# Performance work log

Measured on AMD Instinct MI355X. Metric: run time of the kernel, lower is better.

The kernel has to match this reference:

```python
import jax, jax.numpy as jnp
import numpy as np

QMAX = 127.0
QMIN = -128.0
THRESHOLD = 5e-07

def setup_inputs() -> dict:
    key = jax.random.key(0)
    k1, k2, k3 = jax.random.split(key, 3)
    B, S, Din, Dout = 4, 2048, 4096, 4096
    x = jax.random.normal(k1, (B, S, Din), dtype=jnp.float32)
    # Emulate QuantizedLinear.__init__: per-output-channel symmetric int8 weight quant
    w_fp = jax.random.normal(k2, (Dout, Din), dtype=jnp.float32) * 0.02
    w_scale = jnp.clip(jnp.max(jnp.abs(w_fp), axis=1, keepdims=True), THRESHOLD, None) / QMAX  # [Dout,1]
    weight = jnp.round(w_fp / w_scale)  # int8-valued, stored float32, [Dout, Din]
    weight_scale = w_scale.reshape(1, 1, Dout)  # [1,1,Dout]
    bias = jax.random.normal(k3, (Dout,), dtype=jnp.float32) * 0.01
    return {"x": x, "weight": weight, "weight_scale": weight_scale, "bias": bias}

def reference(x, weight, weight_scale, bias):
    # Dynamic per-tensor activation quantization (act_quant=True, no fixed range)
    fp_min = jnp.min(x)
    fp_max = jnp.max(x)
    scale = (fp_max - fp_min) / (QMAX - QMIN)
    zero_point = jnp.clip(jnp.round(QMIN - fp_min / scale), QMIN, QMAX)
    q_input = jnp.round(x / scale + zero_point)  # int8-valued float
    # F.linear(q_input - zp, weight): [B,S,Din] x [Dout,Din]^T -> [B,S,Dout]
    y = jnp.einsum('bsd,od->bso', q_input - zero_point, weight)
    y = y * scale * weight_scale  # dequant epilogue (weight_scale broadcasts [1,1,Dout])
    return y + bias
```

## Files before the change

kernel.cpp:

```cpp
#include <hip/hip_runtime.h>
#include <hip/hip_bf16.h>
#include <stdint.h>

typedef __attribute__((ext_vector_type(4))) int i32x4;

#define K_DIM 4096
#define M_DIM 8192
#define N_DIM 4096

#define BM 256
#define BN 256
#define BKB 128
#define K_TILES (K_DIM / BKB)
#define GITERS (K_TILES / 2)

__device__ __forceinline__ void gload_lds16(const void* g, void* l) {
    __builtin_amdgcn_global_load_lds(
        (__attribute__((address_space(1))) void*)(void*)g,
        (__attribute__((address_space(3))) void*)(void*)l,
        16, 0, 0);
}

__global__ void mmcw_kernel(const float* __restrict__ x, long n4,
                            float* __restrict__ partials,
                            const float* __restrict__ w,
                            signed char* __restrict__ Wq,
                            int* __restrict__ rowsum) {
    if (blockIdx.x < 1024) {
        const float4* x4 = (const float4*)x;
        float mn = 1e30f, mx = -1e30f;
        long stride = (long)1024 * blockDim.x;
        for (long i = (long)blockIdx.x * blockDim.x + threadIdx.x; i < n4; i += stride) {
            float4 v = x4[i];
            mn = fminf(mn, fminf(fminf(v.x, v.y), fminf(v.z, v.w)));
            mx = fmaxf(mx, fmaxf(fmaxf(v.x, v.y), fmaxf(v.z, v.w)));
        }
        #pragma unroll
        for (int off = 32; off; off >>= 1) {
            mn = fminf(mn, __shfl_down(mn, off));
            mx = fmaxf(mx, __shfl_down(mx, off));
        }
        __shared__ float smn[4], smx[4];
        int wid = threadIdx.x >> 6, lane = threadIdx.x & 63;
        if (lane == 0) { smn[wid] = mn; smx[wid] = mx; }
        __syncthreads();
        if (threadIdx.x == 0) {
            mn = fminf(fminf(smn[0], smn[1]), fminf(smn[2], smn[3]));
            mx = fmaxf(fmaxf(smx[0], smx[1]), fmaxf(smx[2], smx[3]));
            partials[blockIdx.x] = mn;
            partials[1024 + blockIdx.x] = mx;
        }
    } else {
        int row = (blockIdx.x - 1024) * 4 + (threadIdx.x >> 6);
        int lane = threadIdx.x & 63;
        const float4* src = (const float4*)(w + (long)row * K_DIM);
        uint4* dst = (uint4*)(Wq + (long)row * K_DIM);
        float s = 0.f;
        #pragma unroll
        for (int k = 0; k < 4; k++) {
            int u = k * 64 + lane;
            unsigned wrd[4];
            #pragma unroll
            for (int j = 0; j < 4; j++) {
                float4 v = src[u * 4 + j];
                float e[4] = {v.x, v.y, v.z, v.w};
                unsigned word = 0;
                #pragma unroll
                for (int b = 0; b < 4; b++) {
                    int iv = (int)e[b];
                    s += e[b];
                    word |= ((unsigned)iv & 0xffu) << (8 * b);
                }
                wrd[j] = word;
            }
            uint4 o; o.x = wrd[0]; o.y = wrd[1]; o.z = wrd[2]; o.w = wrd[3];
            dst[u] = o;
        }
        #pragma unroll
        for (int off = 32; off; off >>= 1) s += __shfl_down(s, off);
        if (lane == 0) rowsum[row] = (int)s;
    }
}

__global__ void quantize_kernel(const float* __restrict__ x,
                                const float* __restrict__ partials,
                                uint4* __restrict__ q, long n16) {
    float mn = 1e30f, mx = -1e30f;
    for (int i = threadIdx.x; i < 1024; i += 256) {
        mn = fminf(mn, partials[i]);
        mx = fmaxf(mx, partials[1024 + i]);
    }
    #pragma unroll
    for (int off = 32; off; off >>= 1) {
        mn = fminf(mn, __shfl_down(mn, off));
        mx = fmaxf(mx, __shfl_down(mx, off));
    }
    __shared__ float smn[4], smx[4];
    int wid = threadIdx.x >> 6, lane = threadIdx.x & 63;
    if (lane == 0) { smn[wid] = mn; smx[wid] = mx; }
    __syncthreads();
    mn = fminf(fminf(smn[0], smn[1]), fminf(smn[2], smn[3]));
    mx = fmaxf(fmaxf(smx[0], smx[1]), fmaxf(smx[2], smx[3]));
    float scale = (mx - mn) / 255.0f;
    float zp = rintf(-128.0f - mn / scale);
    zp = fminf(fmaxf(zp, -128.0f), 127.0f);

    long stride = (long)gridDim.x * blockDim.x;
    for (long i = (long)blockIdx.x * blockDim.x + threadIdx.x; i < n16; i += stride) {
        const float4* xp = (const float4*)x + i * 4;
        unsigned wrd[4];
        #pragma unroll
        for (int w = 0; w < 4; w++) {
            float4 v = xp[w];
            float e[4] = {v.x, v.y, v.z, v.w};
            unsigned word = 0;
            #pragma unroll
            for (int j = 0; j < 4; j++) {
                float qf = rintf(e[j] / scale + zp);
                qf = fminf(fmaxf(qf, -128.0f), 127.0f);
                int iq = (int)qf;
                word |= ((unsigned)iq & 0xffu) << (8 * j);
            }
            wrd[w] = word;
        }
        uint4 o; o.x = wrd[0]; o.y = wrd[1]; o.z = wrd[2]; o.w = wrd[3];
        q[i] = o;
    }
}

__global__ __launch_bounds__(512, 2) void gemm_kernel(
    const signed char* __restrict__ A,
    const signed char* __restrict__ W,
    const float* __restrict__ partials,
    const int* __restrict__ rowsum,
    const float* __restrict__ wscale,
    const float* __restrict__ bias,
    float* __restrict__ C) {
    extern __shared__ char lds[];
    char* As = lds;
    char* Bs = lds + 65536;

    int nwg = gridDim.x;
    int cpx = nwg >> 3;
    int bid = blockIdx.x;
    int wg = (bid & 7) * cpx + (bid >> 3);
    int tm = wg >> 4;
    int tn = wg & 15;
    int m0 = tm * BM, n0 = tn * BN;

    int t = threadIdx.x;
    int wid = t >> 6, lane = t & 63;
    int wr = wid >> 2, wc = wid & 3;
    int lr = lane & 15, lk = lane >> 4;
    int ksw0 = (lk ^ (lr & 7)) * 16;
    int ksw1 = ((4 + lk) ^ (lr & 7)) * 16;

    int R0 = t >> 3;
    int csw = ((t & 7) ^ ((t >> 3) & 7)) * 16;
    const signed char* aSrc = A + (long)(m0 + R0) * K_DIM + csw;
    const signed char* bSrc = W + (long)(n0 + ((R0 >> 5) << 6) + (R0 & 31)) * K_DIM + csw;
    int ldd = t * 16;

#define STAGE_A(BUF, UN, KT) do { \
    const signed char* _s = aSrc + (long)(UN) * 64 * K_DIM + (long)(KT) * BKB; \
    char* _d = As + (BUF) * 32768 + (UN) * 16384 + ldd; \
    gload_lds16(_s, _d); \
    gload_lds16(_s + (long)128 * K_DIM, _d + 8192); } while (0)

#define STAGE_B(BUF, UN, KT) do { \
    const signed char* _s = bSrc + (long)(UN) * 32 * K_DIM + (long)(KT) * BKB; \
    char* _d = Bs + (BUF) * 32768 + (UN) * 16384 + ldd; \
    gload_lds16(_s, _d); \
    gload_lds16(_s + (long)128 * K_DIM, _d + 8192); } while (0)

#define READ_A(BUF, MH) do { \
    const char* _p = As + (BUF) * 32768 + (MH) * 16384 + (wr * 64 + lr) * 128; \
    _Pragma("unroll") \
    for (int _mm = 0; _mm < 4; ++_mm) { \
        a[_mm * 2]     = *(const i32x4*)(_p + _mm * 2048 + ksw0); \
        a[_mm * 2 + 1] = *(const i32x4*)(_p + _mm * 2048 + ksw1); } } while (0)

#define READ_B(BUF, NH, BR) do { \
    const char* _p = Bs + (BUF) * 32768 + (NH) * 16384 + (wc * 32 + lr) * 128; \
    _Pragma("unroll") \
    for (int _nn = 0; _nn < 2; ++_nn) { \
        BR[_nn * 2]     = *(const i32x4*)(_p + _nn * 2048 + ksw0); \
        BR[_nn * 2 + 1] = *(const i32x4*)(_p + _nn * 2048 + ksw1); } } while (0)

#define MFMA_QUAD(MH, NH, BR) do { \
    _Pragma("unroll") \
    for (int _mm = 0; _mm < 4; ++_mm) \
    _Pragma("unroll") \
    for (int _nn = 0; _nn < 2; ++_nn) { \
        acc[(MH) * 4 + _mm][(NH) * 2 + _nn] = __builtin_amdgcn_mfma_i32_16x16x64_i8( \
            a[_mm * 2], BR[_nn * 2], acc[(MH) * 4 + _mm][(NH) * 2 + _nn], 0, 0, 0); \
        acc[(MH) * 4 + _mm][(NH) * 2 + _nn] = __builtin_amdgcn_mfma_i32_16x16x64_i8( \
            a[_mm * 2 + 1], BR[_nn * 2 + 1], acc[(MH) * 4 + _mm][(NH) * 2 + _nn], 0, 0, 0); } } while (0)

#define BAR()   asm volatile("s_barrier" ::: "memory")
#define LGKM0() asm volatile("s_waitcnt lgkmcnt(0)" ::: "memory")
#define LGKM8() asm volatile("s_waitcnt lgkmcnt(8)" ::: "memory")
#define VM6()   asm volatile("s_waitcnt vmcnt(6)" ::: "memory")
#define VM0()   asm volatile("s_waitcnt vmcnt(0)" ::: "memory")
#define PRIO1() __builtin_amdgcn_s_setprio(1)
#define PRIO0() __builtin_amdgcn_s_setprio(0)

    i32x4 acc[8][4];
    #pragma unroll
    for (int i = 0; i < 8; i++)
        #pragma unroll
        for (int j = 0; j < 4; j++)
            acc[i][j] = (i32x4){0, 0, 0, 0};

    i32x4 a[8], b0[4], b1[4];

    STAGE_A(0, 0, 0); STAGE_B(0, 0, 0); STAGE_B(0, 1, 0); STAGE_A(0, 1, 0);
    STAGE_A(1, 0, 1); STAGE_B(1, 0, 1); STAGE_B(1, 1, 1);
    VM6();
    BAR();

    for (int it = 0; it < GITERS; ++it) {
        int t1 = 2 * it + 1;
        int tn0 = 2 * it + 2, tn1 = 2 * it + 3;
        bool st = (it < GITERS - 1);

        READ_A(0, 0);
        READ_B(0, 0, b0);
        STAGE_A(1, 1, t1);
        LGKM8();
        BAR(); LGKM0();
        PRIO1(); MFMA_QUAD(0, 0, b0); PRIO0();
        BAR();

        READ_B(0, 1, b1);
        if (st) STAGE_A(0, 0, tn0);
        BAR(); LGKM0();
        PRIO1(); MFMA_QUAD(0, 1, b1); PRIO0();
        BAR();

        READ_A(0, 1);
        if (st) STAGE_B(0, 0, tn0);
        BAR(); LGKM0();
        PRIO1(); MFMA_QUAD(1, 1, b1); PRIO0();
        BAR();

        if (st) { STAGE_B(0, 1, tn0); VM6(); } else { VM0(); }
        BAR();
        PRIO1(); MFMA_QUAD(1, 0, b0); PRIO0();
        BAR();

        READ_A(1, 0);
        READ_B(1, 0, b0);
        if (st) STAGE_A(0, 1, tn0);
        LGKM8();
        BAR(); LGKM0();
        PRIO1(); MFMA_QUAD(0, 0, b0); PRIO0();
        BAR();

        READ_B(1, 1, b1);
        if (st) STAGE_A(1, 0, tn1);
        BAR(); LGKM0();
        PRIO1(); MFMA_QUAD(0, 1, b1); PRIO0();
        BAR();

        READ_A(1, 1);
        if (st) STAGE_B(1, 0, tn1);
        BAR(); LGKM0();
        PRIO1(); MFMA_QUAD(1, 1, b1); PRIO0();
        BAR();

        if (st) { STAGE_B(1, 1, tn1); VM6(); }
        BAR();
        PRIO1(); MFMA_QUAD(1, 0, b0); PRIO0();
        BAR();
    }

    float mn = 1e30f, mx = -1e30f;
    for (int i = t; i < 1024; i += 512) {
        mn = fminf(mn, partials[i]);
        mx = fmaxf(mx, partials[1024 + i]);
    }
    #pragma unroll
    for (int off = 32; off; off >>= 1) {
        mn = fminf(mn, __shfl_down(mn, off));
        mx = fmaxf(mx, __shfl_down(mx, off));
    }
    float* red = (float*)lds;
    __syncthreads();
    if (lane == 0) { red[wid] = mn; red[8 + wid] = mx; }
    __syncthreads();
    mn = red[0]; mx = red[8];
    #pragma unroll
    for (int i = 1; i < 8; i++) {
        mn = fminf(mn, red[i]);
        mx = fmaxf(mx, red[8 + i]);
    }
    float scale = (mx - mn) / 255.0f;
    float zp = rintf(-128.0f - mn / scale);
    zp = fminf(fmaxf(zp, -128.0f), 127.0f);

    #pragma unroll
    for (int j = 0; j < 4; j++) {
        int col = n0 + wc * 64 + j * 16 + lr;
        float os = scale * wscale[col];
        float bs = bias[col] - zp * (float)rowsum[col] * os;
        #pragma unroll
        for (int i = 0; i < 8; i++) {
            int rbase = m0 + wr * 128 + i * 16 + lk * 4;
            #pragma unroll
            for (int r = 0; r < 4; r++) {
                C[(long)(rbase + r) * N_DIM + col] = (float)acc[i][j][r] * os + bs;
            }
        }
    }
#undef STAGE_A
#undef STAGE_B
#undef READ_A
#undef READ_B
#undef MFMA_QUAD
}

extern "C" void kernel_launch(void* const* d_in, const int* in_sizes, int n_in,
                              void* d_out, int out_size, void* d_ws, size_t ws_size,
                              hipStream_t stream) {
    const float* x      = (const float*)d_in[0];
    const float* weight = (const float*)d_in[1];
    const float* wscale = (const float*)d_in[2];
    const float* bias   = (const float*)d_in[3];
    float* out = (float*)d_out;

    char* ws = (char*)d_ws;
    signed char* Aq = (signed char*)ws;
    signed char* Wq = (signed char*)(ws + (size_t)32 * 1024 * 1024);
    float* partials = (float*)(ws + (size_t)48 * 1024 * 1024);
    int*   rowsum   = (int*)(partials + 2048);

    long n_x = (long)M_DIM * K_DIM;

    mmcw_kernel<<<2048, 256, 0, stream>>>(x, n_x / 4, partials, weight, Wq, rowsum);
    quantize_kernel<<<2048, 256, 0, stream>>>(x, partials, (uint4*)Aq, n_x / 16);

    int lds_bytes = 131072;
    (void)hipFuncSetAttribute((const void*)gemm_kernel,
                              hipFuncAttributeMaxDynamicSharedMemorySize,
                              lds_bytes);
    dim3 grid((M_DIM / BM) * (N_DIM / BN));
    gemm_kernel<<<grid, 512, lds_bytes, stream>>>(Aq, Wq, partials, rowsum,
                                                  wscale, bias, out);
}
```

Measured before the change: 197.7 us.

## Shrink GEMM tile to 256x128x64 with simple double-buffered pipeline

Replaces the 256x256x128 int8 GEMM tile and its hand-interleaved eight-phase schedule with a 256x128 tile, K-step of 64, and a plain two-stage double-buffered loop: read fragments, barrier, prefetch the tile two steps ahead, then run the MFMAs. LDS use drops from 128KB to 48KB and launch bounds allow 4 blocks per CU, aiming for more occupancy and simpler latency hiding. In exchange each block reuses less data per load, so global/LDS traffic per MFMA rises, and there are more barriers per unit of work.

Result: slower. 225.2 us (+13.9%).

```diff
diff --git a/kernel.cpp b/kernel.cpp
--- a/kernel.cpp
+++ b/kernel.cpp
@@ -9,10 +9,9 @@
 #define N_DIM 4096
 
 #define BM 256
-#define BN 256
-#define BKB 128
+#define BN 128
+#define BKB 64
 #define K_TILES (K_DIM / BKB)
-#define GITERS (K_TILES / 2)
 
 __device__ __forceinline__ void gload_lds16(const void* g, void* l) {
     __builtin_amdgcn_global_load_lds(
@@ -128,7 +127,7 @@
     }
 }
 
-__global__ __launch_bounds__(512, 2) void gemm_kernel(
+__global__ __launch_bounds__(512, 4) void gemm_kernel(
     const signed char* __restrict__ A,
     const signed char* __restrict__ W,
     const float* __restrict__ partials,
@@ -138,140 +137,82 @@
     float* __restrict__ C) {
     extern __shared__ char lds[];
     char* As = lds;
-    char* Bs = lds + 65536;
+    char* Bs = lds + 32768;
 
     int nwg = gridDim.x;
     int cpx = nwg >> 3;
     int bid = blockIdx.x;
     int wg = (bid & 7) * cpx + (bid >> 3);
-    int tm = wg >> 4;
-    int tn = wg & 15;
+    int tm = wg >> 5;
+    int tn = wg & 31;
     int m0 = tm * BM, n0 = tn * BN;
 
     int t = threadIdx.x;
     int wid = t >> 6, lane = t & 63;
-    int wr = wid >> 2, wc = wid & 3;
+    int wr = wid >> 1, wc = wid & 1;
     int lr = lane & 15, lk = lane >> 4;
-    int ksw0 = (lk ^ (lr & 7)) * 16;
-    int ksw1 = ((4 + lk) ^ (lr & 7)) * 16;
-
-    int R0 = t >> 3;
-    int csw = ((t & 7) ^ ((t >> 3) & 7)) * 16;
-    const signed char* aSrc = A + (long)(m0 + R0) * K_DIM + csw;
-    const signed char* bSrc = W + (long)(n0 + ((R0 >> 5) << 6) + (R0 & 31)) * K_DIM + csw;
+    int slot = (lk ^ ((lr >> 1) & 3)) * 16;
+
+    int r0 = t >> 2;
+    int csw = ((t & 3) ^ ((t >> 3) & 3)) * 16;
+    const signed char* aSrc = A + (long)(m0 + r0) * K_DIM + csw;
+    const signed char* bSrc = W + (long)(n0 + r0) * K_DIM + csw;
     int ldd = t * 16;
 
-#define STAGE_A(BUF, UN, KT) do { \
-    const signed char* _s = aSrc + (long)(UN) * 64 * K_DIM + (long)(KT) * BKB; \
-    char* _d = As + (BUF) * 32768 + (UN) * 16384 + ldd; \
-    gload_lds16(_s, _d); \
-    gload_lds16(_s + (long)128 * K_DIM, _d + 8192); } while (0)
-
-#define STAGE_B(BUF, UN, KT) do { \
-    const signed char* _s = bSrc + (long)(UN) * 32 * K_DIM + (long)(KT) * BKB; \
-    char* _d = Bs + (BUF) * 32768 + (UN) * 16384 + ldd; \
-    gload_lds16(_s, _d); \
-    gload_lds16(_s + (long)128 * K_DIM, _d + 8192); } while (0)
-
-#define READ_A(BUF, MH) do { \
-    const char* _p = As + (BUF) * 32768 + (MH) * 16384 + (wr * 64 + lr) * 128; \
-    _Pragma("unroll") \
-    for (int _mm = 0; _mm < 4; ++_mm) { \
-        a[_mm * 2]     = *(const i32x4*)(_p + _mm * 2048 + ksw0); \
-        a[_mm * 2 + 1] = *(const i32x4*)(_p + _mm * 2048 + ksw1); } } while (0)
-
-#define READ_B(BUF, NH, BR) do { \
-    const char* _p = Bs + (BUF) * 32768 + (NH) * 16384 + (wc * 32 + lr) * 128; \
-    _Pragma("unroll") \
-    for (int _nn = 0; _nn < 2; ++_nn) { \
-        BR[_nn * 2]     = *(const i32x4*)(_p + _nn * 2048 + ksw0); \
-        BR[_nn * 2 + 1] = *(const i32x4*)(_p + _nn * 2048 + ksw1); } } while (0)
-
-#define MFMA_QUAD(MH, NH, BR) do { \
-    _Pragma("unroll") \
-    for (int _mm = 0; _mm < 4; ++_mm) \
-    _Pragma("unroll") \
-    for (int _nn = 0; _nn < 2; ++_nn) { \
-        acc[(MH) * 4 + _mm][(NH) * 2 + _nn] = __builtin_amdgcn_mfma_i32_16x16x64_i8( \
-            a[_mm * 2], BR[_nn * 2], acc[(MH) * 4 + _mm][(NH) * 2 + _nn], 0, 0, 0); \
-        acc[(MH) * 4 + _mm][(NH) * 2 + _nn] = __builtin_amdgcn_mfma_i32_16x16x64_i8( \
-            a[_mm * 2 + 1], BR[_nn * 2 + 1], acc[(MH) * 4 + _mm][(NH) * 2 + _nn], 0, 0, 0); } } while (0)
+#define STAGE(BUF, KT) do { \
+    const signed char* _sa = aSrc + (long)(KT) * BKB; \
+    char* _da = As + (BUF) * 16384 + ldd; \
+    gload_lds16(_sa, _da); \
+    gload_lds16(_sa + (long)128 * K_DIM, _da + 8192); \
+    gload_lds16(bSrc + (long)(KT) * BKB, Bs + (BUF) * 8192 + ldd); } while (0)
 
 #define BAR()   asm volatile("s_barrier" ::: "memory")
 #define LGKM0() asm volatile("s_waitcnt lgkmcnt(0)" ::: "memory")
-#define LGKM8() asm volatile("s_waitcnt lgkmcnt(8)" ::: "memory")
-#define VM6()   asm volatile("s_waitcnt vmcnt(6)" ::: "memory")
+#define VM3()   asm volatile("s_waitcnt vmcnt(3)" ::: "memory")
 #define VM0()   asm volatile("s_waitcnt vmcnt(0)" ::: "memory")
 #define PRIO1() __builtin_amdgcn_s_setprio(1)
 #define PRIO0() __builtin_amdgcn_s_setprio(0)
 
-    i32x4 acc[8][4];
-    #pragma unroll
-    for (int i = 0; i < 8; i++)
+    i32x4 acc[4][4];
+    #pragma unroll
+    for (int i = 0; i < 4; i++)
         #pragma unroll
         for (int j = 0; j < 4; j++)
             acc[i][j] = (i32x4){0, 0, 0, 0};
 
-    i32x4 a[8], b0[4], b1[4];
-
-    STAGE_A(0, 0, 0); STAGE_B(0, 0, 0); STAGE_B(0, 1, 0); STAGE_A(0, 1, 0);
-    STAGE_A(1, 0, 1); STAGE_B(1, 0, 1); STAGE_B(1, 1, 1);
-    VM6();
+    i32x4 a[4], b[4];
+
+    STAGE(0, 0);
+    STAGE(1, 1);
+    VM3();
     BAR();
 
-    for (int it = 0; it < GITERS; ++it) {
-        int t1 = 2 * it + 1;
-        int tn0 = 2 * it + 2, tn1 = 2 * it + 3;
-        bool st = (it < GITERS - 1);
-
-        READ_A(0, 0);
-        READ_B(0, 0, b0);
-        STAGE_A(1, 1, t1);
-        LGKM8();
-        BAR(); LGKM0();
-        PRIO1(); MFMA_QUAD(0, 0, b0); PRIO0();
+    int arow = (wr * 64 + lr) * 64 + slot;
+    int brow = (wc * 64 + lr) * 64 + slot;
+
+    for (int kt = 0; kt < K_TILES; ++kt) {
+        int cur = kt & 1;
+        const char* as = As + cur * 16384;
+        const char* bs = Bs + cur * 8192;
+        #pragma unroll
+        for (int mf = 0; mf < 4; ++mf)
+            a[mf] = *(const i32x4*)(as + arow + mf * 1024);
+        #pragma unroll
+        for (int nf = 0; nf < 4; ++nf)
+            b[nf] = *(const i32x4*)(bs + brow + nf * 1024);
+        LGKM0();
         BAR();
-
-        READ_B(0, 1, b1);
-        if (st) STAGE_A(0, 0, tn0);
-        BAR(); LGKM0();
-        PRIO1(); MFMA_QUAD(0, 1, b1); PRIO0();
-        BAR();
-
-        READ_A(0, 1);
-        if (st) STAGE_B(0, 0, tn0);
-        BAR(); LGKM0();
-        PRIO1(); MFMA_QUAD(1, 1, b1); PRIO0();
-        BAR();
-
-        if (st) { STAGE_B(0, 1, tn0); VM6(); } else { VM0(); }
-        BAR();
-        PRIO1(); MFMA_QUAD(1, 0, b0); PRIO0();
-        BAR();
-
-        READ_A(1, 0);
-        READ_B(1, 0, b0);
-        if (st) STAGE_A(0, 1, tn0);
-        LGKM8();
-        BAR(); LGKM0();
-        PRIO1(); MFMA_QUAD(0, 0, b0); PRIO0();
-        BAR();
-
-        READ_B(1, 1, b1);
-        if (st) STAGE_A(1, 0, tn1);
-        BAR(); LGKM0();
-        PRIO1(); MFMA_QUAD(0, 1, b1); PRIO0();
-        BAR();
-
-        READ_A(1, 1);
-        if (st) STAGE_B(1, 0, tn1);
-        BAR(); LGKM0();
-        PRIO1(); MFMA_QUAD(1, 1, b1); PRIO0();
-        BAR();
-
-        if (st) { STAGE_B(1, 1, tn1); VM6(); }
-        BAR();
-        PRIO1(); MFMA_QUAD(1, 0, b0); PRIO0();
+        if (kt < K_TILES - 2) STAGE(cur, kt + 2);
+        PRIO1();
+        #pragma unroll
+        for (int mf = 0; mf < 4; ++mf)
+            #pragma unroll
+            for (int nf = 0; nf < 4; ++nf)
+                acc[mf][nf] = __builtin_amdgcn_mfma_i32_16x16x64_i8(
+                    a[mf], b[nf], acc[mf][nf], 0, 0, 0);
+        PRIO0();
+        if (kt < K_TILES - 2) VM3();
+        else if (kt == K_TILES - 2) VM0();
         BAR();
     }
 
@@ -300,24 +241,20 @@
     zp = fminf(fmaxf(zp, -128.0f), 127.0f);
 
     #pragma unroll
-    for (int j = 0; j < 4; j++) {
-        int col = n0 + wc * 64 + j * 16 + lr;
+    for (int nf = 0; nf < 4; ++nf) {
+        int col = n0 + wc * 64 + nf * 16 + lr;
         float os = scale * wscale[col];
         float bs = bias[col] - zp * (float)rowsum[col] * os;
         #pragma unroll
-        for (int i = 0; i < 8; i++) {
-            int rbase = m0 + wr * 128 + i * 16 + lk * 4;
+        for (int mf = 0; mf < 4; ++mf) {
+            int rbase = m0 + wr * 64 + mf * 16 + lk * 4;
             #pragma unroll
             for (int r = 0; r < 4; r++) {
-                C[(long)(rbase + r) * N_DIM + col] = (float)acc[i][j][r] * os + bs;
+                C[(long)(rbase + r) * N_DIM + col] = (float)acc[mf][nf][r] * os + bs;
             }
         }
     }
-#undef STAGE_A
-#undef STAGE_B
-#undef READ_A
-#undef READ_B
-#undef MFMA_QUAD
+#undef STAGE
 }
 
 extern "C" void kernel_launch(void* const* d_in, const int* in_sizes, int n_in,
@@ -340,7 +277,7 @@
     mmcw_kernel<<<2048, 256, 0, stream>>>(x, n_x / 4, partials, weight, Wq, rowsum);
     quantize_kernel<<<2048, 256, 0, stream>>>(x, partials, (uint4*)Aq, n_x / 16);
 
-    int lds_bytes = 131072;
+    int lds_bytes = 49152;
     (void)hipFuncSetAttribute((const void*)gemm_kernel,
                               hipFuncAttributeMaxDynamicSharedMemorySize,
                               lds_bytes);
```

## Load A operand directly from global into registers, stage only B in LDS

Applied to the files above, without the earlier changes.

The int8 GEMM no longer stages the activation (A) tile through LDS. Each wave now loads its A fragments straight from global memory into registers, interleaved with the MFMA quads, while only the weight (B) tile is double-buffered in LDS with four 16-byte async copies per stage. This halves the LDS footprint and removes the LDS write/read round-trip and the waits tied to A. In exchange, A is fetched redundantly by the four column waves and its global load latency is hidden only by a single MFMA quad, which may stall the pipeline.

New measurement: 403.7 us. 2.04x slower.

```diff
diff --git a/kernel.cpp b/kernel.cpp
--- a/kernel.cpp
+++ b/kernel.cpp
@@ -137,8 +137,7 @@
     const float* __restrict__ bias,
     float* __restrict__ C) {
     extern __shared__ char lds[];
-    char* As = lds;
-    char* Bs = lds + 65536;
+    char* Bs = lds;
 
     int nwg = gridDim.x;
     int cpx = nwg >> 3;
@@ -155,37 +154,33 @@
     int ksw0 = (lk ^ (lr & 7)) * 16;
     int ksw1 = ((4 + lk) ^ (lr & 7)) * 16;
 
-    int R0 = t >> 3;
     int csw = ((t & 7) ^ ((t >> 3) & 7)) * 16;
-    const signed char* aSrc = A + (long)(m0 + R0) * K_DIM + csw;
-    const signed char* bSrc = W + (long)(n0 + ((R0 >> 5) << 6) + (R0 & 31)) * K_DIM + csw;
+    const signed char* bSrc = W + (long)(n0 + (t >> 3)) * K_DIM + csw;
     int ldd = t * 16;
 
-#define STAGE_A(BUF, UN, KT) do { \
-    const signed char* _s = aSrc + (long)(UN) * 64 * K_DIM + (long)(KT) * BKB; \
-    char* _d = As + (BUF) * 32768 + (UN) * 16384 + ldd; \
-    gload_lds16(_s, _d); \
-    gload_lds16(_s + (long)128 * K_DIM, _d + 8192); } while (0)
-
-#define STAGE_B(BUF, UN, KT) do { \
-    const signed char* _s = bSrc + (long)(UN) * 32 * K_DIM + (long)(KT) * BKB; \
-    char* _d = Bs + (BUF) * 32768 + (UN) * 16384 + ldd; \
-    gload_lds16(_s, _d); \
-    gload_lds16(_s + (long)128 * K_DIM, _d + 8192); } while (0)
-
-#define READ_A(BUF, MH) do { \
-    const char* _p = As + (BUF) * 32768 + (MH) * 16384 + (wr * 64 + lr) * 128; \
-    _Pragma("unroll") \
-    for (int _mm = 0; _mm < 4; ++_mm) { \
-        a[_mm * 2]     = *(const i32x4*)(_p + _mm * 2048 + ksw0); \
-        a[_mm * 2 + 1] = *(const i32x4*)(_p + _mm * 2048 + ksw1); } } while (0)
+    const signed char* aBase = A + (long)(m0 + wr * 128 + lr) * K_DIM + lk * 16;
+
+#define STAGE_B(BUF, KT) do { \
+    const signed char* _s = bSrc + (long)(KT) * BKB; \
+    char* _d = Bs + (BUF) * 32768 + ldd; \
+    gload_lds16(_s,                      _d); \
+    gload_lds16(_s + (long) 64 * K_DIM,  _d + 8192); \
+    gload_lds16(_s + (long)128 * K_DIM,  _d + 16384); \
+    gload_lds16(_s + (long)192 * K_DIM,  _d + 24576); } while (0)
 
 #define READ_B(BUF, NH, BR) do { \
-    const char* _p = Bs + (BUF) * 32768 + (NH) * 16384 + (wc * 32 + lr) * 128; \
+    const char* _p = Bs + (BUF) * 32768 + (wc * 64 + (NH) * 32 + lr) * 128; \
     _Pragma("unroll") \
     for (int _nn = 0; _nn < 2; ++_nn) { \
         BR[_nn * 2]     = *(const i32x4*)(_p + _nn * 2048 + ksw0); \
         BR[_nn * 2 + 1] = *(const i32x4*)(_p + _nn * 2048 + ksw1); } } while (0)
+
+#define LOAD_A(MH, KT) do { \
+    const signed char* _p = aBase + (long)(MH) * 64 * K_DIM + (long)(KT) * BKB; \
+    _Pragma("unroll") \
+    for (int _f = 0; _f < 4; ++_f) { \
+        a[_f * 2]     = *(const i32x4*)(_p + (long)_f * 16 * K_DIM); \
+        a[_f * 2 + 1] = *(const i32x4*)(_p + (long)_f * 16 * K_DIM + 64); } } while (0)
 
 #define MFMA_QUAD(MH, NH, BR) do { \
     _Pragma("unroll") \
@@ -199,8 +194,6 @@
 
 #define BAR()   asm volatile("s_barrier" ::: "memory")
 #define LGKM0() asm volatile("s_waitcnt lgkmcnt(0)" ::: "memory")
-#define LGKM8() asm volatile("s_waitcnt lgkmcnt(8)" ::: "memory")
-#define VM6()   asm volatile("s_waitcnt vmcnt(6)" ::: "memory")
 #define VM0()   asm volatile("s_waitcnt vmcnt(0)" ::: "memory")
 #define PRIO1() __builtin_amdgcn_s_setprio(1)
 #define PRIO0() __builtin_amdgcn_s_setprio(0)
@@ -214,64 +207,58 @@
 
     i32x4 a[8], b0[4], b1[4];
 
-    STAGE_A(0, 0, 0); STAGE_B(0, 0, 0); STAGE_B(0, 1, 0); STAGE_A(0, 1, 0);
-    STAGE_A(1, 0, 1); STAGE_B(1, 0, 1); STAGE_B(1, 1, 1);
-    VM6();
+    STAGE_B(0, 0);
+    STAGE_B(1, 1);
+    LOAD_A(0, 0);
+    VM0();
     BAR();
 
     for (int it = 0; it < GITERS; ++it) {
-        int t1 = 2 * it + 1;
+        int te = 2 * it, to = 2 * it + 1;
         int tn0 = 2 * it + 2, tn1 = 2 * it + 3;
         bool st = (it < GITERS - 1);
 
-        READ_A(0, 0);
         READ_B(0, 0, b0);
-        STAGE_A(1, 1, t1);
-        LGKM8();
         BAR(); LGKM0();
         PRIO1(); MFMA_QUAD(0, 0, b0); PRIO0();
         BAR();
 
         READ_B(0, 1, b1);
-        if (st) STAGE_A(0, 0, tn0);
         BAR(); LGKM0();
         PRIO1(); MFMA_QUAD(0, 1, b1); PRIO0();
-        BAR();
-
-        READ_A(0, 1);
-        if (st) STAGE_B(0, 0, tn0);
-        BAR(); LGKM0();
+        LOAD_A(1, te);
+        BAR();
+
+        if (st) STAGE_B(0, tn0);
+        BAR();
         PRIO1(); MFMA_QUAD(1, 1, b1); PRIO0();
         BAR();
 
-        if (st) { STAGE_B(0, 1, tn0); VM6(); } else { VM0(); }
         BAR();
         PRIO1(); MFMA_QUAD(1, 0, b0); PRIO0();
-        BAR();
-
-        READ_A(1, 0);
+        LOAD_A(0, to);
+        BAR();
+
         READ_B(1, 0, b0);
-        if (st) STAGE_A(0, 1, tn0);
-        LGKM8();
         BAR(); LGKM0();
         PRIO1(); MFMA_QUAD(0, 0, b0); PRIO0();
         BAR();
 
         READ_B(1, 1, b1);
-        if (st) STAGE_A(1, 0, tn1);
         BAR(); LGKM0();
         PRIO1(); MFMA_QUAD(0, 1, b1); PRIO0();
-        BAR();
-
-        READ_A(1, 1);
-        if (st) STAGE_B(1, 0, tn1);
-        BAR(); LGKM0();
+        LOAD_A(1, to);
+        BAR();
+
+        if (st) STAGE_B(1, tn1);
+        BAR();
         PRIO1(); MFMA_QUAD(1, 1, b1); PRIO0();
         BAR();
 
-        if (st) { STAGE_B(1, 1, tn1); VM6(); }
+        if (st) VM0();
         BAR();
         PRIO1(); MFMA_QUAD(1, 0, b0); PRIO0();
+        if (st) LOAD_A(0, tn0);
         BAR();
     }
 
@@ -313,10 +300,9 @@
             }
         }
     }
-#undef STAGE_A
 #undef STAGE_B
-#undef READ_A
 #undef READ_B
+#undef LOAD_A
 #undef MFMA_QUAD
 }
 
@@ -340,7 +326,7 @@
     mmcw_kernel<<<2048, 256, 0, stream>>>(x, n_x / 4, partials, weight, Wq, rowsum);
     quantize_kernel<<<2048, 256, 0, stream>>>(x, partials, (uint4*)Aq, n_x / 16);
 
-    int lds_bytes = 131072;
+    int lds_bytes = 65536;
     (void)hipFuncSetAttribute((const void*)gemm_kernel,
                               hipFuncAttributeMaxDynamicSharedMemorySize,
                               lds_bytes);
```
